# Optimization experiments

Measured on AMD Instinct MI355X. Metric: run time of the kernel, lower is better.

## Reference

```python
import jax, jax.numpy as jnp
import numpy as np

N_NODES = 10000
N_EDGES = 320000
IN_FEATS = 512
N_UNITS = 256
OUT_FEATS = 64
N_LAYERS = 6  # number of hidden GCNConv layers feeding the JK max


def setup_inputs() -> dict:
    key = jax.random.key(0)
    ks = jax.random.split(key, 8)
    h = jax.random.normal(ks[0], (N_NODES, IN_FEATS), dtype=jnp.float32)
    edge_index = jax.random.randint(ks[1], (2, N_EDGES), 0, N_NODES, dtype=jnp.int64)
    # learned parameters (glorot-ish scale)
    W0 = jax.random.normal(ks[2], (IN_FEATS, N_UNITS), dtype=jnp.float32) * (1.0 / np.sqrt(IN_FEATS))
    b0 = jnp.zeros((N_UNITS,), dtype=jnp.float32)
    Wh = jax.random.normal(ks[3], (N_LAYERS - 1, N_UNITS, N_UNITS), dtype=jnp.float32) * (1.0 / np.sqrt(N_UNITS))
    bh = jnp.zeros((N_LAYERS - 1, N_UNITS), dtype=jnp.float32)
    Wo = jax.random.normal(ks[4], (N_UNITS, OUT_FEATS), dtype=jnp.float32) * (1.0 / np.sqrt(N_UNITS))
    bo = jnp.zeros((OUT_FEATS,), dtype=jnp.float32)
    return {"h": h, "edge_index": edge_index, "W0": W0, "b0": b0,
            "Wh": Wh, "bh": bh, "Wo": Wo, "bo": bo}


def reference(h, edge_index, W0, b0, Wh, bh, Wo, bo):
    src = edge_index[0]
    dst = edge_index[1]
    n = h.shape[0]

    def conv_plain(x, W, b):
        # GCNConv with normalize=False: plain sum aggregation over edges, no self-loops
        m = x @ W                                   # [N, d]
        agg = jax.ops.segment_sum(m[src], dst, num_segments=n)
        return jax.nn.relu(agg + b)

    outs = []
    x = conv_plain(h, W0, b0)
    outs.append(x)
    for i in range(Wh.shape[0]):  # dropout is identity in eval mode
        x = conv_plain(x, Wh[i], bh[i])
        outs.append(x)

    # jumping-knowledge max aggregation over layer outputs
    x = jnp.max(jnp.stack(outs, axis=0), axis=0)    # [N, n_units]

    # final GCNConv with normalize=True (symmetric GCN norm, self-loops added)
    m = x @ Wo                                      # [N, out_feats]
    ones = jnp.ones(dst.shape, dtype=m.dtype)
    deg = jax.ops.segment_sum(ones, dst, num_segments=n) + 1.0  # +1 self loop
    dinv = deg ** -0.5
    coef = dinv[src] * dinv[dst]                    # [E]
    agg = jax.ops.segment_sum(m[src] * coef[:, None], dst, num_segments=n)
    agg = agg + m / deg[:, None] + bo               # self-loop term 1/deg_i
    return jax.nn.log_softmax(agg, axis=-1)
```

## Files before the change

### kernel.cpp

```cpp
#include <hip/hip_runtime.h>
#include <math.h>

#define N_NODES 10000
#define N_EDGES 320000
#define IN_FEATS 512
#define N_UNITS 256
#define OUT_FEATS 64
#define N_HID 5

typedef __attribute__((ext_vector_type(8))) short bf16x8;
typedef __attribute__((ext_vector_type(4))) float f32x4;

__device__ __forceinline__ unsigned short f2bf(float f) {
    union { float f; unsigned int u; } c; c.f = f;
    unsigned int u = c.u + 0x7FFFu + ((c.u >> 16) & 1u);
    return (unsigned short)(u >> 16);
}
__device__ __forceinline__ float bf2f(unsigned int b) {
    union { unsigned int u; float f; } c; c.u = (b & 0xffffu) << 16;
    return c.f;
}


__global__ void k_setup(const int* __restrict__ dst, int* __restrict__ deg,
                        const float* __restrict__ h, unsigned short* __restrict__ hb,
                        const float* __restrict__ W0, const float* __restrict__ Wh,
                        const float* __restrict__ Wo,
                        unsigned short* __restrict__ W0t, unsigned short* __restrict__ Wht,
                        unsigned short* __restrict__ Wot) {
    const int R1 = N_EDGES;
    const int R2 = N_NODES * IN_FEATS / 4;
    const int S0 = IN_FEATS * N_UNITS;
    const int SH = N_HID * N_UNITS * N_UNITS;
    const int SO = N_UNITS * OUT_FEATS;
    int t = blockIdx.x * blockDim.x + threadIdx.x;
    if (t < R1) {
        atomicAdd(&deg[dst[t]], 1);
    } else if (t < R1 + R2) {
        int u = t - R1;
        float4 v = reinterpret_cast<const float4*>(h)[u];
        ushort4 o;
        o.x = f2bf(v.x); o.y = f2bf(v.y); o.z = f2bf(v.z); o.w = f2bf(v.w);
        reinterpret_cast<ushort4*>(hb)[u] = o;
    } else {
        int u = t - R1 - R2;
        if (u < S0) {
            int k = u >> 8, n = u & 255;
            W0t[(size_t)n * IN_FEATS + k] = f2bf(W0[u]);
        } else if (u < S0 + SH) {
            int w = u - S0;
            int l = w >> 16;
            int r = w & 65535;
            int k = r >> 8, n = r & 255;
            Wht[(size_t)l * 65536 + (size_t)n * N_UNITS + k] = f2bf(Wh[w]);
        } else if (u < S0 + SH + SO) {
            int w = u - S0 - SH;
            int k = w >> 6, n = w & 63;
            Wot[(size_t)n * N_UNITS + k] = f2bf(Wo[w]);
        }
    }
}


__global__ __launch_bounds__(1024) void k_scan(const int* __restrict__ deg,
                                               int* __restrict__ row_ptr,
                                               int* __restrict__ cursor,
                                               float* __restrict__ dinv,
                                               float* __restrict__ invdeg) {
    __shared__ int wsum[16];
    const int PER = 10;
    int t = threadIdx.x;
    int lane = t & 63, wid = t >> 6;
    int base = t * PER;

    int v[PER];
    int s = 0;
#pragma unroll
    for (int j = 0; j < PER; ++j) {
        int i = base + j;
        int d = (i < N_NODES) ? deg[i] : 0;
        v[j] = s;
        s += d;
    }
    int inc = s;
#pragma unroll
    for (int off = 1; off < 64; off <<= 1) {
        int y = __shfl_up(inc, off);
        if (lane >= off) inc += y;
    }
    if (lane == 63) wsum[wid] = inc;
    __syncthreads();
    if (wid == 0) {
        int w = (lane < 16) ? wsum[lane] : 0;
#pragma unroll
        for (int off = 1; off < 16; off <<= 1) {
            int y = __shfl_up(w, off);
            if (lane >= off) w += y;
        }
        if (lane < 16) wsum[lane] = w;
    }
    __syncthreads();
    int wave_excl = (wid == 0) ? 0 : wsum[wid - 1];
    int thread_excl = wave_excl + (inc - s);

#pragma unroll
    for (int j = 0; j < PER; ++j) {
        int i = base + j;
        if (i < N_NODES) {
            int rp = thread_excl + v[j];
            row_ptr[i] = rp;
            cursor[i]  = rp;
            int d = ((j + 1 < PER) ? v[j + 1] : s) - v[j];
            float dd = (float)(d + 1);
            dinv[i]   = rsqrtf(dd);
            invdeg[i] = 1.0f / dd;
        }
    }
    if (t == 1023) row_ptr[N_NODES] = thread_excl + s;
}

__global__ void k_fill(const int* __restrict__ src, const int* __restrict__ dst,
                       int* __restrict__ cursor, int* __restrict__ csr_src) {
    int e = blockIdx.x * blockDim.x + threadIdx.x;
    if (e < N_EDGES) {
        int p = atomicAdd(&cursor[dst[e]], 1);
        csr_src[p] = src[e];
    }
}


__global__ __launch_bounds__(256) void k_mgemm(const unsigned short* __restrict__ A,
                                               const unsigned short* __restrict__ Bt,
                                               unsigned short* __restrict__ C,
                                               const int M, const int K, const int Nld) {
    constexpr int BM = 64, BN = 64, BK = 32;
    __shared__ unsigned short As[2][BM * BK];
    __shared__ unsigned short Bs[2][BN * BK];

    const int tid  = threadIdx.x;
    const int wid  = tid >> 6;
    const int lane = tid & 63;
    const int wr   = wid >> 1;
    const int wc   = wid & 1;
    const int brow = blockIdx.x * BM;
    const int bcol = blockIdx.y * BN;

    const int lr = lane & 15;
    const int lk = lane >> 4;

    const int row  = tid >> 2;
    const int slot = tid & 3;
    const int sslot = slot ^ ((row >> 1) & 3);

    int gra = brow + row; if (gra >= M) gra = M - 1;
    const unsigned short* gpa = A + (size_t)gra * K + sslot * 8;
    const unsigned short* gpb = Bt + (size_t)(bcol + row) * K + sslot * 8;

    f32x4 acc[2][2];
#pragma unroll
    for (int m = 0; m < 2; ++m)
#pragma unroll
        for (int n = 0; n < 2; ++n)
            acc[m][n] = (f32x4){0.f, 0.f, 0.f, 0.f};

#define STAGE(buf, k0)                                                                      \
    do {                                                                                    \
        __builtin_amdgcn_global_load_lds(                                                   \
            (const __attribute__((address_space(1))) void*)(gpa + (k0)),                    \
            (__attribute__((address_space(3))) void*)(&As[(buf)][tid * 8]), 16, 0, 0);      \
        __builtin_amdgcn_global_load_lds(                                                   \
            (const __attribute__((address_space(1))) void*)(gpb + (k0)),                    \
            (__attribute__((address_space(3))) void*)(&Bs[(buf)][tid * 8]), 16, 0, 0);      \
    } while (0)

    STAGE(0, 0);
    __syncthreads();

    const int nk = K / BK;
    for (int kt = 0; kt < nk; ++kt) {
        const int cur = kt & 1;
        if (kt + 1 < nk) STAGE(cur ^ 1, (kt + 1) * BK);

        bf16x8 af[2], bfr[2];
#pragma unroll
        for (int m = 0; m < 2; ++m) {
            int ra = wr * 32 + m * 16 + lr;
            af[m] = *reinterpret_cast<const bf16x8*>(&As[cur][ra * BK + (lk ^ ((ra >> 1) & 3)) * 8]);
        }
#pragma unroll
        for (int n = 0; n < 2; ++n) {
            int rb = wc * 32 + n * 16 + lr;
            bfr[n] = *reinterpret_cast<const bf16x8*>(&Bs[cur][rb * BK + (lk ^ ((rb >> 1) & 3)) * 8]);
        }
#pragma unroll
        for (int m = 0; m < 2; ++m)
#pragma unroll
            for (int n = 0; n < 2; ++n)
                acc[m][n] = __builtin_amdgcn_mfma_f32_16x16x32_bf16(af[m], bfr[n], acc[m][n], 0, 0, 0);
        __syncthreads();
    }
#undef STAGE

#pragma unroll
    for (int m = 0; m < 2; ++m) {
#pragma unroll
        for (int r = 0; r < 4; ++r) {
            int orow = brow + wr * 32 + m * 16 + lk * 4 + r;
            if (orow < M) {
#pragma unroll
                for (int n = 0; n < 2; ++n) {
                    int ocol = bcol + wc * 32 + n * 16 + lr;
                    C[(size_t)orow * Nld + ocol] = f2bf(acc[m][n][r]);
                }
            }
        }
    }
}


__global__ __launch_bounds__(256) void k_wgemm(const unsigned short* __restrict__ A,
                                               const unsigned short* __restrict__ Bt,
                                               unsigned short* __restrict__ C,
                                               const int M, const int Nld) {
    constexpr int K = 256;
    __shared__ unsigned short As[64 * K];
    __shared__ unsigned short Bs[64 * K];

    const int tid  = threadIdx.x;
    const int wid  = tid >> 6;
    const int lane = tid & 63;
    const int lr   = lane & 15;
    const int lk   = lane >> 4;
    const int brow = blockIdx.x * 64;
    const int bcol = blockIdx.y * 64;

#pragma unroll
    for (int p = 0; p < 8; ++p) {
        int i = p * 256 + tid;
        int row = i >> 5, s = i & 31;
        int gr = brow + row; if (gr >= M) gr = M - 1;
        const unsigned short* gp = A + (size_t)gr * K + ((s ^ (row & 7)) * 8);
        __builtin_amdgcn_global_load_lds(
            (const __attribute__((address_space(1))) void*)gp,
            (__attribute__((address_space(3))) void*)(As + i * 8), 16, 0, 0);
    }
#pragma unroll
    for (int p = 0; p < 8; ++p) {
        int i = p * 256 + tid;
        int row = i >> 5, s = i & 31;
        const unsigned short* gp = Bt + (size_t)(bcol + row) * K + ((s ^ (row & 7)) * 8);
        __builtin_amdgcn_global_load_lds(
            (const __attribute__((address_space(1))) void*)gp,
            (__attribute__((address_space(3))) void*)(Bs + i * 8), 16, 0, 0);
    }
    __syncthreads();

    f32x4 acc[4];
#pragma unroll
    for (int n = 0; n < 4; ++n) acc[n] = (f32x4){0.f, 0.f, 0.f, 0.f};

    const int ra = (wid << 4) + lr;
    const unsigned short* Arow = As + ra * K;
    const int e = lr & 7;
#pragma unroll
    for (int kk = 0; kk < 8; ++kk) {
        bf16x8 av = *reinterpret_cast<const bf16x8*>(&Arow[(((kk << 2) + lk) ^ e) * 8]);
#pragma unroll
        for (int n = 0; n < 4; ++n) {
            const unsigned short* Brow = Bs + ((n << 4) + lr) * K;
            bf16x8 bv = *reinterpret_cast<const bf16x8*>(&Brow[(((kk << 2) + lk) ^ e) * 8]);
            acc[n] = __builtin_amdgcn_mfma_f32_16x16x32_bf16(av, bv, acc[n], 0, 0, 0);
        }
    }

#pragma unroll
    for (int n = 0; n < 4; ++n) {
#pragma unroll
        for (int r = 0; r < 4; ++r) {
            int orow = brow + (wid << 4) + (lk << 2) + r;
            if (orow < M) {
                int ocol = bcol + (n << 4) + lr;
                C[(size_t)orow * Nld + ocol] = f2bf(acc[n][r]);
            }
        }
    }
}


__global__ __launch_bounds__(256) void k_agg(const unsigned short* __restrict__ m,
                                             const int* __restrict__ row_ptr,
                                             const int* __restrict__ csr_src,
                                             const float* __restrict__ bias,
                                             unsigned short* __restrict__ x_out,
                                             unsigned short* __restrict__ jk,
                                             int init_jk) {
    int half = threadIdx.x >> 5;
    int lane = threadIdx.x & 31;
    int n = blockIdx.x * 8 + half;
    int s = row_ptr[n], e = row_ptr[n + 1];
    const uint4* mv = (const uint4*)m;

    float a[8];
#pragma unroll
    for (int j = 0; j < 8; ++j) a[j] = 0.f;

#define ACC8(u)                                        \
    do {                                               \
        a[0] += bf2f((u).x); a[1] += bf2f((u).x >> 16);\
        a[2] += bf2f((u).y); a[3] += bf2f((u).y >> 16);\
        a[4] += bf2f((u).z); a[5] += bf2f((u).z >> 16);\
        a[6] += bf2f((u).w); a[7] += bf2f((u).w >> 16);\
    } while (0)

    int i = s;
    for (; i + 3 < e; i += 4) {
        int s0 = csr_src[i], s1 = csr_src[i + 1], s2 = csr_src[i + 2], s3 = csr_src[i + 3];
        uint4 u0 = mv[(size_t)s0 * 32 + lane];
        uint4 u1 = mv[(size_t)s1 * 32 + lane];
        uint4 u2 = mv[(size_t)s2 * 32 + lane];
        uint4 u3 = mv[(size_t)s3 * 32 + lane];
        ACC8(u0); ACC8(u1); ACC8(u2); ACC8(u3);
    }
    for (; i < e; ++i) {
        uint4 u = mv[(size_t)csr_src[i] * 32 + lane];
        ACC8(u);
    }
#undef ACC8

    float4 b0 = ((const float4*)bias)[lane * 2];
    float4 b1 = ((const float4*)bias)[lane * 2 + 1];
    unsigned int hh[8];
    hh[0] = f2bf(fmaxf(a[0] + b0.x, 0.f));
    hh[1] = f2bf(fmaxf(a[1] + b0.y, 0.f));
    hh[2] = f2bf(fmaxf(a[2] + b0.z, 0.f));
    hh[3] = f2bf(fmaxf(a[3] + b0.w, 0.f));
    hh[4] = f2bf(fmaxf(a[4] + b1.x, 0.f));
    hh[5] = f2bf(fmaxf(a[5] + b1.y, 0.f));
    hh[6] = f2bf(fmaxf(a[6] + b1.z, 0.f));
    hh[7] = f2bf(fmaxf(a[7] + b1.w, 0.f));
    uint4 o;
    o.x = hh[0] | (hh[1] << 16);
    o.y = hh[2] | (hh[3] << 16);
    o.z = hh[4] | (hh[5] << 16);
    o.w = hh[6] | (hh[7] << 16);

    size_t idx = (size_t)n * 32 + lane;
    ((uint4*)x_out)[idx] = o;
    if (init_jk) {
        ((uint4*)jk)[idx] = o;
    } else {
        uint4 j = ((const uint4*)jk)[idx];
        auto mx2 = [](unsigned int nw, unsigned int od) {
            unsigned int lo_n = nw & 0xffffu, lo_o = od & 0xffffu;
            unsigned int hi_n = nw >> 16,     hi_o = od >> 16;
            unsigned int lo = lo_n > lo_o ? lo_n : lo_o;
            unsigned int hi = hi_n > hi_o ? hi_n : hi_o;
            return lo | (hi << 16);
        };
        uint4 w;
        w.x = mx2(o.x, j.x); w.y = mx2(o.y, j.y);
        w.z = mx2(o.z, j.z); w.w = mx2(o.w, j.w);
        ((uint4*)jk)[idx] = w;
    }
}


__global__ __launch_bounds__(256) void k_final(const unsigned short* __restrict__ mf,
                                               const int* __restrict__ row_ptr,
                                               const int* __restrict__ csr_src,
                                               const float* __restrict__ dinv,
                                               const float* __restrict__ invdeg,
                                               const float* __restrict__ bo,
                                               float* __restrict__ out) {
    int wid  = threadIdx.x >> 6;
    int lane = threadIdx.x & 63;
    int n = blockIdx.x * 4 + wid;
    if (n >= N_NODES) return;

    int s = row_ptr[n], e = row_ptr[n + 1];
    float acc = 0.f;
    int i = s;
    for (; i + 3 < e; i += 4) {
        int s0 = csr_src[i], s1 = csr_src[i + 1], s2 = csr_src[i + 2], s3 = csr_src[i + 3];
        acc += bf2f(mf[(size_t)s0 * OUT_FEATS + lane]) * dinv[s0];
        acc += bf2f(mf[(size_t)s1 * OUT_FEATS + lane]) * dinv[s1];
        acc += bf2f(mf[(size_t)s2 * OUT_FEATS + lane]) * dinv[s2];
        acc += bf2f(mf[(size_t)s3 * OUT_FEATS + lane]) * dinv[s3];
    }
    for (; i < e; ++i) {
        int sr = csr_src[i];
        acc += bf2f(mf[(size_t)sr * OUT_FEATS + lane]) * dinv[sr];
    }
    acc *= dinv[n];
    acc += bf2f(mf[(size_t)n * OUT_FEATS + lane]) * invdeg[n] + bo[lane];

    float mx = acc;
#pragma unroll
    for (int off = 32; off; off >>= 1) mx = fmaxf(mx, __shfl_xor(mx, off));
    float ex = __expf(acc - mx);
    float sum = ex;
#pragma unroll
    for (int off = 32; off; off >>= 1) sum += __shfl_xor(sum, off);
    out[(size_t)n * OUT_FEATS + lane] = acc - mx - __logf(sum);
}


extern "C" void kernel_launch(void* const* d_in, const int* in_sizes, int n_in,
                              void* d_out, int out_size, void* d_ws, size_t ws_size,
                              hipStream_t stream) {
    const float* h  = (const float*)d_in[0];
    const int*   ei = (const int*)d_in[1];
    const float* W0 = (const float*)d_in[2];
    const float* b0 = (const float*)d_in[3];
    const float* Wh = (const float*)d_in[4];
    const float* bh = (const float*)d_in[5];
    const float* Wo = (const float*)d_in[6];
    const float* bo = (const float*)d_in[7];

    const int* src = ei;
    const int* dst = ei + N_EDGES;

    char* p = (char*)d_ws;
    auto carve = [&](size_t bytes) {
        char* r = p;
        p += (bytes + 255) & ~(size_t)255;
        return r;
    };
    int*   deg     = (int*)  carve(N_NODES * 4);
    int*   row_ptr = (int*)  carve((N_NODES + 1) * 4);
    int*   cursor  = (int*)  carve(N_NODES * 4);
    int*   csr_src = (int*)  carve(N_EDGES * 4);
    float* dinv    = (float*)carve(N_NODES * 4);
    float* invdeg  = (float*)carve(N_NODES * 4);
    unsigned short* hb  = (unsigned short*)carve((size_t)N_NODES * IN_FEATS * 2);
    unsigned short* W0t = (unsigned short*)carve((size_t)IN_FEATS * N_UNITS * 2);
    unsigned short* Wht = (unsigned short*)carve((size_t)N_HID * N_UNITS * N_UNITS * 2);
    unsigned short* Wot = (unsigned short*)carve((size_t)N_UNITS * OUT_FEATS * 2);
    unsigned short* m   = (unsigned short*)carve((size_t)N_NODES * N_UNITS * 2);
    unsigned short* x   = (unsigned short*)carve((size_t)N_NODES * N_UNITS * 2);
    unsigned short* jk  = (unsigned short*)carve((size_t)N_NODES * N_UNITS * 2);
    unsigned short* mf  = (unsigned short*)carve((size_t)N_NODES * OUT_FEATS * 2);

    hipMemsetAsync(deg, 0, N_NODES * 4, stream);
    {
        const int total = N_EDGES + N_NODES * IN_FEATS / 4 +
                          IN_FEATS * N_UNITS + N_HID * N_UNITS * N_UNITS + N_UNITS * OUT_FEATS;
        k_setup<<<(total + 255) / 256, 256, 0, stream>>>(dst, deg, h, hb, W0, Wh, Wo,
                                                         W0t, Wht, Wot);
    }
    k_scan<<<1, 1024, 0, stream>>>(deg, row_ptr, cursor, dinv, invdeg);
    k_fill<<<(N_EDGES + 255) / 256, 256, 0, stream>>>(src, dst, cursor, csr_src);

    const int GBM = (N_NODES + 63) / 64;

    {
        dim3 g(GBM, N_UNITS / 64);
        k_mgemm<<<g, 256, 0, stream>>>(hb, W0t, m, N_NODES, IN_FEATS, N_UNITS);
    }
    k_agg<<<N_NODES / 8, 256, 0, stream>>>(m, row_ptr, csr_src, b0, x, jk, 1);

    for (int l = 0; l < N_HID; ++l) {
        dim3 g(GBM, N_UNITS / 64);
        k_wgemm<<<g, 256, 0, stream>>>(x, Wht + (size_t)l * N_UNITS * N_UNITS, m,
                                       N_NODES, N_UNITS);
        k_agg<<<N_NODES / 8, 256, 0, stream>>>(m, row_ptr, csr_src, bh + (size_t)l * N_UNITS,
                                               x, jk, 0);
    }

    {
        dim3 g(GBM, 1);
        k_wgemm<<<g, 256, 0, stream>>>(jk, Wot, mf, N_NODES, OUT_FEATS);
    }
    k_final<<<(N_NODES + 3) / 4, 256, 0, stream>>>(mf, row_ptr, csr_src, dinv, invdeg,
                                                   bo, (float*)d_out);
}
```

Measured before the change: 258.1 us.

## Reorder each GCN layer to aggregate-then-transform and fuse gather with the MFMA GEMM

Each hidden layer now aggregates neighbour features first (A·X) and then multiplies by W, using linearity, inside one kernel. The gathered 8-node tile goes to LDS and is fed to MFMA, with the weights read straight from global memory. This removes the separate GEMM launches and the intermediate m buffer round-trip. The final layer likewise aggregates the 256-wide JK features with normalisation before a small GEMM fused with log-softmax. The trade-offs are gathering wider rows (512 or 256 features instead of the transformed width), which costs more for layer 0 and the final layer, an MFMA tile half-padded with zeros, and weights reloaded from global/L2 by every block.

```diff
diff --git a/kernel.cpp b/kernel.cpp
--- a/kernel.cpp
+++ b/kernel.cpp
@@ -49,8 +49,7 @@
             W0t[(size_t)n * IN_FEATS + k] = f2bf(W0[u]);
         } else if (u < S0 + SH) {
             int w = u - S0;
-            int l = w >> 16;
-            int r = w & 65535;
+            int l = w >> 16, r = w & 65535;
             int k = r >> 8, n = r & 255;
             Wht[(size_t)l * 65536 + (size_t)n * N_UNITS + k] = f2bf(Wh[w]);
         } else if (u < S0 + SH + SO) {
@@ -129,176 +128,131 @@
 }
 
 
-__global__ __launch_bounds__(256) void k_mgemm(const unsigned short* __restrict__ A,
-                                               const unsigned short* __restrict__ Bt,
-                                               unsigned short* __restrict__ C,
-                                               const int M, const int K, const int Nld) {
-    constexpr int BM = 64, BN = 64, BK = 32;
-    __shared__ unsigned short As[2][BM * BK];
-    __shared__ unsigned short Bs[2][BN * BK];
-
-    const int tid  = threadIdx.x;
-    const int wid  = tid >> 6;
-    const int lane = tid & 63;
-    const int wr   = wid >> 1;
-    const int wc   = wid & 1;
-    const int brow = blockIdx.x * BM;
-    const int bcol = blockIdx.y * BN;
-
-    const int lr = lane & 15;
-    const int lk = lane >> 4;
-
-    const int row  = tid >> 2;
-    const int slot = tid & 3;
-    const int sslot = slot ^ ((row >> 1) & 3);
-
-    int gra = brow + row; if (gra >= M) gra = M - 1;
-    const unsigned short* gpa = A + (size_t)gra * K + sslot * 8;
-    const unsigned short* gpb = Bt + (size_t)(bcol + row) * K + sslot * 8;
-
-    f32x4 acc[2][2];
-#pragma unroll
-    for (int m = 0; m < 2; ++m)
-#pragma unroll
-        for (int n = 0; n < 2; ++n)
-            acc[m][n] = (f32x4){0.f, 0.f, 0.f, 0.f};
-
-#define STAGE(buf, k0)                                                                      \
-    do {                                                                                    \
-        __builtin_amdgcn_global_load_lds(                                                   \
-            (const __attribute__((address_space(1))) void*)(gpa + (k0)),                    \
-            (__attribute__((address_space(3))) void*)(&As[(buf)][tid * 8]), 16, 0, 0);      \
-        __builtin_amdgcn_global_load_lds(                                                   \
-            (const __attribute__((address_space(1))) void*)(gpb + (k0)),                    \
-            (__attribute__((address_space(3))) void*)(&Bs[(buf)][tid * 8]), 16, 0, 0);      \
+__global__ __launch_bounds__(256) void k_l0(const unsigned short* __restrict__ hb,
+                                            const int* __restrict__ row_ptr,
+                                            const int* __restrict__ csr_src,
+                                            const unsigned short* __restrict__ W0t,
+                                            const float* __restrict__ b0,
+                                            unsigned short* __restrict__ x_out,
+                                            unsigned short* __restrict__ jk) {
+    constexpr int K = IN_FEATS;
+    __shared__ unsigned short U[16 * K];
+
+    const int tid = threadIdx.x;
+    const int tg = tid >> 5, sl = tid & 31;
+
+    {
+        uint4 z4 = {0u, 0u, 0u, 0u};
+        ((uint4*)(U + 8 * K))[tid] = z4;
+        ((uint4*)(U + 8 * K))[tid + 256] = z4;
+    }
+
+    const int n = blockIdx.x * 8 + tg;
+    const int s = row_ptr[n], e = row_ptr[n + 1];
+    const uint4* hv = (const uint4*)hb;
+
+    float a[16];
+#pragma unroll
+    for (int j = 0; j < 16; ++j) a[j] = 0.f;
+
+#define ACCL(u, base)                                                        \
+    do {                                                                     \
+        a[base + 0] += bf2f((u).x); a[base + 1] += bf2f((u).x >> 16);        \
+        a[base + 2] += bf2f((u).y); a[base + 3] += bf2f((u).y >> 16);        \
+        a[base + 4] += bf2f((u).z); a[base + 5] += bf2f((u).z >> 16);        \
+        a[base + 6] += bf2f((u).w); a[base + 7] += bf2f((u).w >> 16);        \
     } while (0)
 
-    STAGE(0, 0);
+    int i = s;
+    for (; i + 1 < e; i += 2) {
+        int s0 = csr_src[i], s1 = csr_src[i + 1];
+        uint4 u0 = hv[(size_t)s0 * 64 + sl];
+        uint4 u1 = hv[(size_t)s0 * 64 + 32 + sl];
+        uint4 u2 = hv[(size_t)s1 * 64 + sl];
+        uint4 u3 = hv[(size_t)s1 * 64 + 32 + sl];
+        ACCL(u0, 0); ACCL(u1, 8); ACCL(u2, 0); ACCL(u3, 8);
+    }
+    for (; i < e; ++i) {
+        int sr = csr_src[i];
+        uint4 u0 = hv[(size_t)sr * 64 + sl];
+        uint4 u1 = hv[(size_t)sr * 64 + 32 + sl];
+        ACCL(u0, 0); ACCL(u1, 8);
+    }
+#undef ACCL
+
+    uint4 o0, o1;
+    o0.x = f2bf(a[0]) | ((unsigned)f2bf(a[1]) << 16);
+    o0.y = f2bf(a[2]) | ((unsigned)f2bf(a[3]) << 16);
+    o0.z = f2bf(a[4]) | ((unsigned)f2bf(a[5]) << 16);
+    o0.w = f2bf(a[6]) | ((unsigned)f2bf(a[7]) << 16);
+    o1.x = f2bf(a[8]) | ((unsigned)f2bf(a[9]) << 16);
+    o1.y = f2bf(a[10]) | ((unsigned)f2bf(a[11]) << 16);
+    o1.z = f2bf(a[12]) | ((unsigned)f2bf(a[13]) << 16);
+    o1.w = f2bf(a[14]) | ((unsigned)f2bf(a[15]) << 16);
+    ((uint4*)U)[tg * 64 + (sl ^ tg)] = o0;
+    ((uint4*)U)[tg * 64 + ((32 + sl) ^ tg)] = o1;
     __syncthreads();
 
-    const int nk = K / BK;
-    for (int kt = 0; kt < nk; ++kt) {
-        const int cur = kt & 1;
-        if (kt + 1 < nk) STAGE(cur ^ 1, (kt + 1) * BK);
-
-        bf16x8 af[2], bfr[2];
-#pragma unroll
-        for (int m = 0; m < 2; ++m) {
-            int ra = wr * 32 + m * 16 + lr;
-            af[m] = *reinterpret_cast<const bf16x8*>(&As[cur][ra * BK + (lk ^ ((ra >> 1) & 3)) * 8]);
-        }
-#pragma unroll
-        for (int n = 0; n < 2; ++n) {
-            int rb = wc * 32 + n * 16 + lr;
-            bfr[n] = *reinterpret_cast<const bf16x8*>(&Bs[cur][rb * BK + (lk ^ ((rb >> 1) & 3)) * 8]);
-        }
-#pragma unroll
-        for (int m = 0; m < 2; ++m)
-#pragma unroll
-            for (int n = 0; n < 2; ++n)
-                acc[m][n] = __builtin_amdgcn_mfma_f32_16x16x32_bf16(af[m], bfr[n], acc[m][n], 0, 0, 0);
-        __syncthreads();
-    }
-#undef STAGE
-
-#pragma unroll
-    for (int m = 0; m < 2; ++m) {
-#pragma unroll
-        for (int r = 0; r < 4; ++r) {
-            int orow = brow + wr * 32 + m * 16 + lk * 4 + r;
-            if (orow < M) {
-#pragma unroll
-                for (int n = 0; n < 2; ++n) {
-                    int ocol = bcol + wc * 32 + n * 16 + lr;
-                    C[(size_t)orow * Nld + ocol] = f2bf(acc[m][n][r]);
-                }
+    const int wid = tid >> 6, lane = tid & 63;
+    const int lr = lane & 15, lk = lane >> 4;
+    const unsigned short* Urow = U + lr * K;
+    const int ex = lr & 7;
+
+    f32x4 acc[4];
+#pragma unroll
+    for (int n4 = 0; n4 < 4; ++n4) acc[n4] = (f32x4){0.f, 0.f, 0.f, 0.f};
+
+#pragma unroll
+    for (int kk = 0; kk < K / 32; ++kk) {
+        bf16x8 av = *(const bf16x8*)(Urow + ((((kk << 2) + lk)) ^ ex) * 8);
+#pragma unroll
+        for (int n4 = 0; n4 < 4; ++n4) {
+            const unsigned short* brow =
+                W0t + (size_t)(wid * 64 + n4 * 16 + lr) * K + kk * 32 + lk * 8;
+            bf16x8 bv = *(const bf16x8*)brow;
+            acc[n4] = __builtin_amdgcn_mfma_f32_16x16x32_bf16(av, bv, acc[n4], 0, 0, 0);
+        }
+    }
+
+    if (lk < 2) {
+#pragma unroll
+        for (int n4 = 0; n4 < 4; ++n4) {
+            int col = wid * 64 + n4 * 16 + lr;
+            float bb = b0[col];
+#pragma unroll
+            for (int rr = 0; rr < 4; ++rr) {
+                int node = blockIdx.x * 8 + (lk << 2) + rr;
+                unsigned short v = f2bf(fmaxf(acc[n4][rr] + bb, 0.f));
+                size_t idx = (size_t)node * N_UNITS + col;
+                x_out[idx] = v;
+                jk[idx] = v;
             }
         }
     }
 }
 
 
-__global__ __launch_bounds__(256) void k_wgemm(const unsigned short* __restrict__ A,
-                                               const unsigned short* __restrict__ Bt,
-                                               unsigned short* __restrict__ C,
-                                               const int M, const int Nld) {
-    constexpr int K = 256;
-    __shared__ unsigned short As[64 * K];
-    __shared__ unsigned short Bs[64 * K];
-
-    const int tid  = threadIdx.x;
-    const int wid  = tid >> 6;
-    const int lane = tid & 63;
-    const int lr   = lane & 15;
-    const int lk   = lane >> 4;
-    const int brow = blockIdx.x * 64;
-    const int bcol = blockIdx.y * 64;
-
-#pragma unroll
-    for (int p = 0; p < 8; ++p) {
-        int i = p * 256 + tid;
-        int row = i >> 5, s = i & 31;
-        int gr = brow + row; if (gr >= M) gr = M - 1;
-        const unsigned short* gp = A + (size_t)gr * K + ((s ^ (row & 7)) * 8);
-        __builtin_amdgcn_global_load_lds(
-            (const __attribute__((address_space(1))) void*)gp,
-            (__attribute__((address_space(3))) void*)(As + i * 8), 16, 0, 0);
-    }
-#pragma unroll
-    for (int p = 0; p < 8; ++p) {
-        int i = p * 256 + tid;
-        int row = i >> 5, s = i & 31;
-        const unsigned short* gp = Bt + (size_t)(bcol + row) * K + ((s ^ (row & 7)) * 8);
-        __builtin_amdgcn_global_load_lds(
-            (const __attribute__((address_space(1))) void*)gp,
-            (__attribute__((address_space(3))) void*)(Bs + i * 8), 16, 0, 0);
-    }
-    __syncthreads();
-
-    f32x4 acc[4];
-#pragma unroll
-    for (int n = 0; n < 4; ++n) acc[n] = (f32x4){0.f, 0.f, 0.f, 0.f};
-
-    const int ra = (wid << 4) + lr;
-    const unsigned short* Arow = As + ra * K;
-    const int e = lr & 7;
-#pragma unroll
-    for (int kk = 0; kk < 8; ++kk) {
-        bf16x8 av = *reinterpret_cast<const bf16x8*>(&Arow[(((kk << 2) + lk) ^ e) * 8]);
-#pragma unroll
-        for (int n = 0; n < 4; ++n) {
-            const unsigned short* Brow = Bs + ((n << 4) + lr) * K;
-            bf16x8 bv = *reinterpret_cast<const bf16x8*>(&Brow[(((kk << 2) + lk) ^ e) * 8]);
-            acc[n] = __builtin_amdgcn_mfma_f32_16x16x32_bf16(av, bv, acc[n], 0, 0, 0);
-        }
-    }
-
-#pragma unroll
-    for (int n = 0; n < 4; ++n) {
-#pragma unroll
-        for (int r = 0; r < 4; ++r) {
-            int orow = brow + (wid << 4) + (lk << 2) + r;
-            if (orow < M) {
-                int ocol = bcol + (n << 4) + lr;
-                C[(size_t)orow * Nld + ocol] = f2bf(acc[n][r]);
-            }
-        }
-    }
-}
-
-
-__global__ __launch_bounds__(256) void k_agg(const unsigned short* __restrict__ m,
-                                             const int* __restrict__ row_ptr,
-                                             const int* __restrict__ csr_src,
-                                             const float* __restrict__ bias,
-                                             unsigned short* __restrict__ x_out,
-                                             unsigned short* __restrict__ jk,
-                                             int init_jk) {
-    int half = threadIdx.x >> 5;
-    int lane = threadIdx.x & 31;
-    int n = blockIdx.x * 8 + half;
-    int s = row_ptr[n], e = row_ptr[n + 1];
-    const uint4* mv = (const uint4*)m;
+__global__ __launch_bounds__(256) void k_lh(const unsigned short* __restrict__ x_in,
+                                            const int* __restrict__ row_ptr,
+                                            const int* __restrict__ csr_src,
+                                            const unsigned short* __restrict__ Wt,
+                                            const float* __restrict__ bias,
+                                            unsigned short* __restrict__ x_out,
+                                            unsigned short* __restrict__ jk) {
+    constexpr int K = N_UNITS;
+    __shared__ unsigned short U[16 * K];
+
+    const int tid = threadIdx.x;
+    const int tg = tid >> 5, sl = tid & 31;
+
+    {
+        uint4 z4 = {0u, 0u, 0u, 0u};
+        ((uint4*)(U + 8 * K))[tid] = z4;
+    }
+
+    const int n = blockIdx.x * 8 + tg;
+    const int s = row_ptr[n], e = row_ptr[n + 1];
+    const uint4* xv = (const uint4*)x_in;
 
     float a[8];
 #pragma unroll
@@ -314,94 +268,198 @@
 
     int i = s;
     for (; i + 3 < e; i += 4) {
-        int s0 = csr_src[i], s1 = csr_src[i + 1], s2 = csr_src[i + 2], s3 = csr_src[i + 3];
-        uint4 u0 = mv[(size_t)s0 * 32 + lane];
-        uint4 u1 = mv[(size_t)s1 * 32 + lane];
-        uint4 u2 = mv[(size_t)s2 * 32 + lane];
-        uint4 u3 = mv[(size_t)s3 * 32 + lane];
+        uint4 u0 = xv[(size_t)csr_src[i + 0] * 32 + sl];
+        uint4 u1 = xv[(size_t)csr_src[i + 1] * 32 + sl];
+        uint4 u2 = xv[(size_t)csr_src[i + 2] * 32 + sl];
+        uint4 u3 = xv[(size_t)csr_src[i + 3] * 32 + sl];
         ACC8(u0); ACC8(u1); ACC8(u2); ACC8(u3);
     }
     for (; i < e; ++i) {
-        uint4 u = mv[(size_t)csr_src[i] * 32 + lane];
+        uint4 u = xv[(size_t)csr_src[i] * 32 + sl];
         ACC8(u);
     }
 #undef ACC8
 
-    float4 b0 = ((const float4*)bias)[lane * 2];
-    float4 b1 = ((const float4*)bias)[lane * 2 + 1];
-    unsigned int hh[8];
-    hh[0] = f2bf(fmaxf(a[0] + b0.x, 0.f));
-    hh[1] = f2bf(fmaxf(a[1] + b0.y, 0.f));
-    hh[2] = f2bf(fmaxf(a[2] + b0.z, 0.f));
-    hh[3] = f2bf(fmaxf(a[3] + b0.w, 0.f));
-    hh[4] = f2bf(fmaxf(a[4] + b1.x, 0.f));
-    hh[5] = f2bf(fmaxf(a[5] + b1.y, 0.f));
-    hh[6] = f2bf(fmaxf(a[6] + b1.z, 0.f));
-    hh[7] = f2bf(fmaxf(a[7] + b1.w, 0.f));
-    uint4 o;
-    o.x = hh[0] | (hh[1] << 16);
-    o.y = hh[2] | (hh[3] << 16);
-    o.z = hh[4] | (hh[5] << 16);
-    o.w = hh[6] | (hh[7] << 16);
-
-    size_t idx = (size_t)n * 32 + lane;
-    ((uint4*)x_out)[idx] = o;
-    if (init_jk) {
-        ((uint4*)jk)[idx] = o;
-    } else {
-        uint4 j = ((const uint4*)jk)[idx];
-        auto mx2 = [](unsigned int nw, unsigned int od) {
-            unsigned int lo_n = nw & 0xffffu, lo_o = od & 0xffffu;
-            unsigned int hi_n = nw >> 16,     hi_o = od >> 16;
-            unsigned int lo = lo_n > lo_o ? lo_n : lo_o;
-            unsigned int hi = hi_n > hi_o ? hi_n : hi_o;
-            return lo | (hi << 16);
-        };
-        uint4 w;
-        w.x = mx2(o.x, j.x); w.y = mx2(o.y, j.y);
-        w.z = mx2(o.z, j.z); w.w = mx2(o.w, j.w);
-        ((uint4*)jk)[idx] = w;
-    }
-}
-
-
-__global__ __launch_bounds__(256) void k_final(const unsigned short* __restrict__ mf,
-                                               const int* __restrict__ row_ptr,
-                                               const int* __restrict__ csr_src,
-                                               const float* __restrict__ dinv,
-                                               const float* __restrict__ invdeg,
-                                               const float* __restrict__ bo,
-                                               float* __restrict__ out) {
-    int wid  = threadIdx.x >> 6;
-    int lane = threadIdx.x & 63;
-    int n = blockIdx.x * 4 + wid;
-    if (n >= N_NODES) return;
-
-    int s = row_ptr[n], e = row_ptr[n + 1];
-    float acc = 0.f;
+    uint4 o0;
+    o0.x = f2bf(a[0]) | ((unsigned)f2bf(a[1]) << 16);
+    o0.y = f2bf(a[2]) | ((unsigned)f2bf(a[3]) << 16);
+    o0.z = f2bf(a[4]) | ((unsigned)f2bf(a[5]) << 16);
+    o0.w = f2bf(a[6]) | ((unsigned)f2bf(a[7]) << 16);
+    ((uint4*)U)[tg * 32 + (sl ^ tg)] = o0;
+    __syncthreads();
+
+    const int wid = tid >> 6, lane = tid & 63;
+    const int lr = lane & 15, lk = lane >> 4;
+    const unsigned short* Urow = U + lr * K;
+    const int ex = lr & 7;
+
+    f32x4 acc[4];
+#pragma unroll
+    for (int n4 = 0; n4 < 4; ++n4) acc[n4] = (f32x4){0.f, 0.f, 0.f, 0.f};
+
+#pragma unroll
+    for (int kk = 0; kk < K / 32; ++kk) {
+        bf16x8 av = *(const bf16x8*)(Urow + ((((kk << 2) + lk)) ^ ex) * 8);
+#pragma unroll
+        for (int n4 = 0; n4 < 4; ++n4) {
+            const unsigned short* brow =
+                Wt + (size_t)(wid * 64 + n4 * 16 + lr) * K + kk * 32 + lk * 8;
+            bf16x8 bv = *(const bf16x8*)brow;
+            acc[n4] = __builtin_amdgcn_mfma_f32_16x16x32_bf16(av, bv, acc[n4], 0, 0, 0);
+        }
+    }
+
+    if (lk < 2) {
+#pragma unroll
+        for (int n4 = 0; n4 < 4; ++n4) {
+            int col = wid * 64 + n4 * 16 + lr;
+            float bb = bias[col];
+#pragma unroll
+            for (int rr = 0; rr < 4; ++rr) {
+                int node = blockIdx.x * 8 + (lk << 2) + rr;
+                unsigned short v = f2bf(fmaxf(acc[n4][rr] + bb, 0.f));
+                size_t idx = (size_t)node * N_UNITS + col;
+                x_out[idx] = v;
+                unsigned short jm = jk[idx];
+                jk[idx] = (v > jm) ? v : jm;
+            }
+        }
+    }
+}
+
+
+__global__ __launch_bounds__(256) void k_zg(const unsigned short* __restrict__ jk,
+                                            const int* __restrict__ row_ptr,
+                                            const int* __restrict__ csr_src,
+                                            const float* __restrict__ dinv,
+                                            const float* __restrict__ invdeg,
+                                            unsigned short* __restrict__ z) {
+    const int tg = threadIdx.x >> 5, sl = threadIdx.x & 31;
+    const int n = blockIdx.x * 8 + tg;
+    const int s = row_ptr[n], e = row_ptr[n + 1];
+    const uint4* jv = (const uint4*)jk;
+
+    float a[8];
+#pragma unroll
+    for (int j = 0; j < 8; ++j) a[j] = 0.f;
+
+#define ACCW(u, d)                                                     \
+    do {                                                               \
+        a[0] += bf2f((u).x) * (d); a[1] += bf2f((u).x >> 16) * (d);    \
+        a[2] += bf2f((u).y) * (d); a[3] += bf2f((u).y >> 16) * (d);    \
+        a[4] += bf2f((u).z) * (d); a[5] += bf2f((u).z >> 16) * (d);    \
+        a[6] += bf2f((u).w) * (d); a[7] += bf2f((u).w >> 16) * (d);    \
+    } while (0)
+
     int i = s;
-    for (; i + 3 < e; i += 4) {
-        int s0 = csr_src[i], s1 = csr_src[i + 1], s2 = csr_src[i + 2], s3 = csr_src[i + 3];
-        acc += bf2f(mf[(size_t)s0 * OUT_FEATS + lane]) * dinv[s0];
-        acc += bf2f(mf[(size_t)s1 * OUT_FEATS + lane]) * dinv[s1];
-        acc += bf2f(mf[(size_t)s2 * OUT_FEATS + lane]) * dinv[s2];
-        acc += bf2f(mf[(size_t)s3 * OUT_FEATS + lane]) * dinv[s3];
+    for (; i + 1 < e; i += 2) {
+        int s0 = csr_src[i], s1 = csr_src[i + 1];
+        uint4 u0 = jv[(size_t)s0 * 32 + sl];
+        uint4 u1 = jv[(size_t)s1 * 32 + sl];
+        float d0 = dinv[s0], d1 = dinv[s1];
+        ACCW(u0, d0); ACCW(u1, d1);
     }
     for (; i < e; ++i) {
         int sr = csr_src[i];
-        acc += bf2f(mf[(size_t)sr * OUT_FEATS + lane]) * dinv[sr];
-    }
-    acc *= dinv[n];
-    acc += bf2f(mf[(size_t)n * OUT_FEATS + lane]) * invdeg[n] + bo[lane];
-
-    float mx = acc;
-#pragma unroll
-    for (int off = 32; off; off >>= 1) mx = fmaxf(mx, __shfl_xor(mx, off));
-    float ex = __expf(acc - mx);
-    float sum = ex;
-#pragma unroll
-    for (int off = 32; off; off >>= 1) sum += __shfl_xor(sum, off);
-    out[(size_t)n * OUT_FEATS + lane] = acc - mx - __logf(sum);
+        uint4 u = jv[(size_t)sr * 32 + sl];
+        float d = dinv[sr];
+        ACCW(u, d);
+    }
+#undef ACCW
+
+    float dn = dinv[n], idg = invdeg[n];
+    uint4 un = jv[(size_t)n * 32 + sl];
+    uint4 o;
+    o.x = f2bf(dn * a[0] + idg * bf2f(un.x)) |
+          ((unsigned)f2bf(dn * a[1] + idg * bf2f(un.x >> 16)) << 16);
+    o.y = f2bf(dn * a[2] + idg * bf2f(un.y)) |
+          ((unsigned)f2bf(dn * a[3] + idg * bf2f(un.y >> 16)) << 16);
+    o.z = f2bf(dn * a[4] + idg * bf2f(un.z)) |
+          ((unsigned)f2bf(dn * a[5] + idg * bf2f(un.z >> 16)) << 16);
+    o.w = f2bf(dn * a[6] + idg * bf2f(un.w)) |
+          ((unsigned)f2bf(dn * a[7] + idg * bf2f(un.w >> 16)) << 16);
+    ((uint4*)z)[(size_t)n * 32 + sl] = o;
+}
+
+
+__global__ __launch_bounds__(256) void k_fg(const unsigned short* __restrict__ z,
+                                            const unsigned short* __restrict__ Wot,
+                                            const float* __restrict__ bo,
+                                            float* __restrict__ out) {
+    constexpr int K = 256;
+    __shared__ unsigned short As[64 * K];
+    __shared__ unsigned short Bs[64 * K];
+
+    const int tid  = threadIdx.x;
+    const int wid  = tid >> 6;
+    const int lane = tid & 63;
+    const int lr   = lane & 15;
+    const int lk   = lane >> 4;
+    const int brow = blockIdx.x * 64;
+
+#pragma unroll
+    for (int p = 0; p < 8; ++p) {
+        int i = p * 256 + tid;
+        int row = i >> 5, s = i & 31;
+        int gr = brow + row; if (gr >= N_NODES) gr = N_NODES - 1;
+        const unsigned short* gp = z + (size_t)gr * K + ((s ^ (row & 7)) * 8);
+        __builtin_amdgcn_global_load_lds(
+            (const __attribute__((address_space(1))) void*)gp,
+            (__attribute__((address_space(3))) void*)(As + i * 8), 16, 0, 0);
+    }
+#pragma unroll
+    for (int p = 0; p < 8; ++p) {
+        int i = p * 256 + tid;
+        int row = i >> 5, s = i & 31;
+        const unsigned short* gp = Wot + (size_t)row * K + ((s ^ (row & 7)) * 8);
+        __builtin_amdgcn_global_load_lds(
+            (const __attribute__((address_space(1))) void*)gp,
+            (__attribute__((address_space(3))) void*)(Bs + i * 8), 16, 0, 0);
+    }
+    __syncthreads();
+
+    f32x4 acc[4];
+#pragma unroll
+    for (int n4 = 0; n4 < 4; ++n4) acc[n4] = (f32x4){0.f, 0.f, 0.f, 0.f};
+
+    const unsigned short* Arow = As + ((wid << 4) + lr) * K;
+    const int ex = lr & 7;
+#pragma unroll
+    for (int kk = 0; kk < 8; ++kk) {
+        bf16x8 av = *(const bf16x8*)(&Arow[(((kk << 2) + lk) ^ ex) * 8]);
+#pragma unroll
+        for (int n4 = 0; n4 < 4; ++n4) {
+            const unsigned short* Brow = Bs + ((n4 << 4) + lr) * K;
+            bf16x8 bv = *(const bf16x8*)(&Brow[(((kk << 2) + lk) ^ ex) * 8]);
+            acc[n4] = __builtin_amdgcn_mfma_f32_16x16x32_bf16(av, bv, acc[n4], 0, 0, 0);
+        }
+    }
+
+    float bb[4];
+#pragma unroll
+    for (int n4 = 0; n4 < 4; ++n4) bb[n4] = bo[n4 * 16 + lr];
+
+#pragma unroll
+    for (int rr = 0; rr < 4; ++rr) {
+        float v0 = acc[0][rr] + bb[0];
+        float v1 = acc[1][rr] + bb[1];
+        float v2 = acc[2][rr] + bb[2];
+        float v3 = acc[3][rr] + bb[3];
+        float mx = fmaxf(fmaxf(v0, v1), fmaxf(v2, v3));
+#pragma unroll
+        for (int off = 8; off; off >>= 1) mx = fmaxf(mx, __shfl_xor(mx, off));
+        float sm = __expf(v0 - mx) + __expf(v1 - mx) + __expf(v2 - mx) + __expf(v3 - mx);
+#pragma unroll
+        for (int off = 8; off; off >>= 1) sm += __shfl_xor(sm, off);
+        float ls = mx + __logf(sm);
+        int orow = brow + (wid << 4) + (lk << 2) + rr;
+        if (orow < N_NODES) {
+            out[(size_t)orow * OUT_FEATS + 0 * 16 + lr] = v0 - ls;
+            out[(size_t)orow * OUT_FEATS + 1 * 16 + lr] = v1 - ls;
+            out[(size_t)orow * OUT_FEATS + 2 * 16 + lr] = v2 - ls;
+            out[(size_t)orow * OUT_FEATS + 3 * 16 + lr] = v3 - ls;
+        }
+    }
 }
 
 
@@ -436,10 +494,10 @@
     unsigned short* W0t = (unsigned short*)carve((size_t)IN_FEATS * N_UNITS * 2);
     unsigned short* Wht = (unsigned short*)carve((size_t)N_HID * N_UNITS * N_UNITS * 2);
     unsigned short* Wot = (unsigned short*)carve((size_t)N_UNITS * OUT_FEATS * 2);
-    unsigned short* m   = (unsigned short*)carve((size_t)N_NODES * N_UNITS * 2);
-    unsigned short* x   = (unsigned short*)carve((size_t)N_NODES * N_UNITS * 2);
+    unsigned short* xa  = (unsigned short*)carve((size_t)N_NODES * N_UNITS * 2);
+    unsigned short* xb  = (unsigned short*)carve((size_t)N_NODES * N_UNITS * 2);
     unsigned short* jk  = (unsigned short*)carve((size_t)N_NODES * N_UNITS * 2);
-    unsigned short* mf  = (unsigned short*)carve((size_t)N_NODES * OUT_FEATS * 2);
+    unsigned short* z   = (unsigned short*)carve((size_t)N_NODES * N_UNITS * 2);
 
     hipMemsetAsync(deg, 0, N_NODES * 4, stream);
     {
@@ -451,26 +509,17 @@
     k_scan<<<1, 1024, 0, stream>>>(deg, row_ptr, cursor, dinv, invdeg);
     k_fill<<<(N_EDGES + 255) / 256, 256, 0, stream>>>(src, dst, cursor, csr_src);
 
-    const int GBM = (N_NODES + 63) / 64;
-
-    {
-        dim3 g(GBM, N_UNITS / 64);
-        k_mgemm<<<g, 256, 0, stream>>>(hb, W0t, m, N_NODES, IN_FEATS, N_UNITS);
-    }
-    k_agg<<<N_NODES / 8, 256, 0, stream>>>(m, row_ptr, csr_src, b0, x, jk, 1);
-
+    k_l0<<<N_NODES / 8, 256, 0, stream>>>(hb, row_ptr, csr_src, W0t, b0, xa, jk);
+
+    unsigned short* cur = xa;
+    unsigned short* nxt = xb;
     for (int l = 0; l < N_HID; ++l) {
-        dim3 g(GBM, N_UNITS / 64);
-        k_wgemm<<<g, 256, 0, stream>>>(x, Wht + (size_t)l * N_UNITS * N_UNITS, m,
-                                       N_NODES, N_UNITS);
-        k_agg<<<N_NODES / 8, 256, 0, stream>>>(m, row_ptr, csr_src, bh + (size_t)l * N_UNITS,
-                                               x, jk, 0);
-    }
-
-    {
-        dim3 g(GBM, 1);
-        k_wgemm<<<g, 256, 0, stream>>>(jk, Wot, mf, N_NODES, OUT_FEATS);
-    }
-    k_final<<<(N_NODES + 3) / 4, 256, 0, stream>>>(mf, row_ptr, csr_src, dinv, invdeg,
-                                                   bo, (float*)d_out);
-}
+        k_lh<<<N_NODES / 8, 256, 0, stream>>>(cur, row_ptr, csr_src,
+                                              Wht + (size_t)l * N_UNITS * N_UNITS,
+                                              bh + (size_t)l * N_UNITS, nxt, jk);
+        unsigned short* t = cur; cur = nxt; nxt = t;
+    }
+
+    k_zg<<<N_NODES / 8, 256, 0, stream>>>(jk, row_ptr, csr_src, dinv, invdeg, z);
+    k_fg<<<(N_NODES + 63) / 64, 256, 0, stream>>>(z, Wot, bo, (float*)d_out);
+}
```

Measured after the change: 346.8 us. +34.4%, slower.
